# Optimization experiments

Measured on AMD Instinct MI355X. Metric: run time of the kernel, lower is better.

The kernel has to match this reference:

```python
import jax, jax.numpy as jnp
import numpy as np

NUM_SEGMENTS = 16

def setup_inputs() -> dict:
    key = jax.random.key(0)
    k1, k2, k3, k4 = jax.random.split(key, 4)
    C, R = 256, 4
    x = jax.random.normal(k1, (1000000, C), dtype=jnp.float32)
    indices = jax.random.randint(k2, (1000000,), 0, NUM_SEGMENTS, dtype=jnp.int64)
    # Linear weights (torch Linear: y = x @ W.T); store as (in, out) for einsum
    w1 = jax.random.normal(k3, (C, C // R), dtype=jnp.float32) / np.sqrt(C)
    w2 = jax.random.normal(k4, (C // R, C), dtype=jnp.float32) / np.sqrt(C // R)
    return {"x": x, "indices": indices, "w1": w1, "w2": w2}

def reference(x, indices, w1, w2):
    idx = indices.astype(jnp.int32)
    # scatter-mean over segments: (S, C)
    seg_sum = jax.ops.segment_sum(x, idx, num_segments=NUM_SEGMENTS)
    counts = jax.ops.segment_sum(jnp.ones((x.shape[0],), x.dtype), idx, num_segments=NUM_SEGMENTS)
    seg_mean = seg_sum / jnp.maximum(counts, 1.0)[:, None]
    # tiny SE MLP: Linear -> ReLU -> Linear -> Sigmoid
    h = jax.nn.relu(seg_mean @ w1)
    gate = jax.nn.sigmoid(h @ w2)  # (S, C)
    # gather per-point gate and modulate
    return x * gate[idx]
```

## Files before the change

### kernel.cpp

```cpp
#include <hip/hip_runtime.h>
#include <math.h>

#define C 256
#define S 16
#define CR 64
#define NREP 16

typedef float f4 __attribute__((ext_vector_type(4)));

__global__ __launch_bounds__(256) void k_hist(
    const int* __restrict__ idx, int* __restrict__ pcnt, int nrows)
{
    const int lane = threadIdx.x & 63;
    const int tid  = blockIdx.x * blockDim.x + threadIdx.x;
    const int T    = gridDim.x * blockDim.x;
    const int padded = ((nrows + 63) >> 6) << 6;

    int c0=0,c1=0,c2=0,c3=0,c4=0,c5=0,c6=0,c7=0,
        c8=0,c9=0,c10=0,c11=0,c12=0,c13=0,c14=0,c15=0;

    for (int i = tid; i < padded; i += T) {
        const int v = (i < nrows) ? idx[i] : -1;
        #define CNT(K) c##K += (int)__popcll(__ballot(v == K));
        CNT(0)  CNT(1)  CNT(2)  CNT(3)  CNT(4)  CNT(5)  CNT(6)  CNT(7)
        CNT(8)  CNT(9)  CNT(10) CNT(11) CNT(12) CNT(13) CNT(14) CNT(15)
        #undef CNT
    }
    if (lane == 0) {
        #define FL(K) if (c##K) atomicAdd(&pcnt[K], c##K);
        FL(0)  FL(1)  FL(2)  FL(3)  FL(4)  FL(5)  FL(6)  FL(7)
        FL(8)  FL(9)  FL(10) FL(11) FL(12) FL(13) FL(14) FL(15)
        #undef FL
    }
}

__global__ __launch_bounds__(256, 4) void k_segsum(
    const float* __restrict__ x, const int* __restrict__ idx,
    float* __restrict__ psum, int nrows)
{
    const int  tid = blockIdx.x * 256 + threadIdx.x;
    const int  T   = gridDim.x * 256;
    const long n4  = (long)nrows * (C / 4);

    f4 a0={0,0,0,0},a1={0,0,0,0},a2={0,0,0,0},a3={0,0,0,0},
       a4={0,0,0,0},a5={0,0,0,0},a6={0,0,0,0},a7={0,0,0,0},
       a8={0,0,0,0},a9={0,0,0,0},a10={0,0,0,0},a11={0,0,0,0},
       a12={0,0,0,0},a13={0,0,0,0},a14={0,0,0,0},a15={0,0,0,0};

    const f4* __restrict__ x4 = reinterpret_cast<const f4*>(x);

    #define ACC1(K, sv, vv) { const float m = (sv == K) ? 1.0f : 0.0f; \
        a##K.x = fmaf(m, vv.x, a##K.x); a##K.y = fmaf(m, vv.y, a##K.y); \
        a##K.z = fmaf(m, vv.z, a##K.z); a##K.w = fmaf(m, vv.w, a##K.w); }
    #define ROW(sv, vv) \
        ACC1(0,sv,vv)  ACC1(1,sv,vv)  ACC1(2,sv,vv)  ACC1(3,sv,vv) \
        ACC1(4,sv,vv)  ACC1(5,sv,vv)  ACC1(6,sv,vv)  ACC1(7,sv,vv) \
        ACC1(8,sv,vv)  ACC1(9,sv,vv)  ACC1(10,sv,vv) ACC1(11,sv,vv) \
        ACC1(12,sv,vv) ACC1(13,sv,vv) ACC1(14,sv,vv) ACC1(15,sv,vv)

    long i = tid;
    for (; i + T < n4; i += 2L * T) {
        const f4  v0 = x4[i];
        const f4  v1 = x4[i + T];
        const int s0 = idx[i >> 6];
        const int s1 = idx[(i + T) >> 6];
        ROW(s0, v0)
        ROW(s1, v1)
    }
    for (; i < n4; i += T) {
        const f4  v = x4[i];
        const int s = idx[i >> 6];
        ROW(s, v)
    }
    #undef ROW
    #undef ACC1

    __shared__ float red[4][8][C];
    const int w    = threadIdx.x >> 6;
    const int lane = threadIdx.x & 63;
    const int t    = threadIdx.x;
    const int rep  = blockIdx.x & (NREP - 1);
    float* gs = psum + (size_t)rep * S * C;

    #define ST(K, SL) *reinterpret_cast<f4*>(&red[w][SL][4 * lane]) = a##K;
    ST(0,0) ST(1,1) ST(2,2) ST(3,3) ST(4,4) ST(5,5) ST(6,6) ST(7,7)
    __syncthreads();
    #pragma unroll
    for (int s_ = 0; s_ < 8; s_++) {
        const float v = red[0][s_][t] + red[1][s_][t] +
                        red[2][s_][t] + red[3][s_][t];
        atomicAdd(&gs[s_ * C + t], v);
    }
    __syncthreads();
    ST(8,0) ST(9,1) ST(10,2) ST(11,3) ST(12,4) ST(13,5) ST(14,6) ST(15,7)
    __syncthreads();
    #pragma unroll
    for (int s_ = 0; s_ < 8; s_++) {
        const float v = red[0][s_][t] + red[1][s_][t] +
                        red[2][s_][t] + red[3][s_][t];
        atomicAdd(&gs[(8 + s_) * C + t], v);
    }
    #undef ST
}

__global__ __launch_bounds__(256) void k_mlp(
    const float* __restrict__ psum, const int* __restrict__ pcnt,
    const float* __restrict__ w1, const float* __restrict__ w2,
    float* __restrict__ gate)
{
    __shared__ float sm[S][C];
    __shared__ float h[S][CR];
    __shared__ float cnt[S];
    const int t = threadIdx.x;

    if (t < S) cnt[t] = fmaxf((float)pcnt[t], 1.0f);
    __syncthreads();

    for (int i = t; i < S * C; i += 256) {
        float v = 0.0f;
        #pragma unroll
        for (int r = 0; r < NREP; r++) v += psum[r * S * C + i];
        sm[i / C][i % C] = v / cnt[i / C];
    }
    __syncthreads();

    for (int o = t; o < S * CR; o += 256) {
        const int s = o / CR, j = o % CR;
        float acc = 0.0f;
        #pragma unroll 4
        for (int k = 0; k < C; k++) acc += sm[s][k] * w1[k * CR + j];
        h[s][j] = fmaxf(acc, 0.0f);
    }
    __syncthreads();

    for (int o = t; o < S * C; o += 256) {
        const int s = o / C, j = o % C;
        float acc = 0.0f;
        #pragma unroll
        for (int k = 0; k < CR; k++) acc += h[s][k] * w2[k * C + j];
        gate[o] = 1.0f / (1.0f + expf(-acc));
    }
}

__global__ __launch_bounds__(256) void k_mod(
    const float* __restrict__ x, const int* __restrict__ idx,
    const float* __restrict__ gate, float* __restrict__ out, int nrows)
{
    const int l    = threadIdx.x & 63;
    const int wrow = threadIdx.x >> 6;
    const float4* __restrict__ x4 = reinterpret_cast<const float4*>(x);
    const float4* __restrict__ g4 = reinterpret_cast<const float4*>(gate);
    float4* __restrict__ o4 = reinterpret_cast<float4*>(out);

    for (int row = blockIdx.x * 4 + wrow; row < nrows; row += gridDim.x * 4) {
        const int s = idx[row];
        float4 v = x4[row * (C / 4) + l];
        const float4 g = g4[s * (C / 4) + l];
        v.x *= g.x; v.y *= g.y; v.z *= g.z; v.w *= g.w;
        o4[row * (C / 4) + l] = v;
    }
}

extern "C" void kernel_launch(void* const* d_in, const int* in_sizes, int n_in,
                              void* d_out, int out_size, void* d_ws, size_t ws_size,
                              hipStream_t stream)
{
    const float* x   = (const float*)d_in[0];
    const int*   idx = (const int*)  d_in[1];
    const float* w1  = (const float*)d_in[2];
    const float* w2  = (const float*)d_in[3];
    float* out = (float*)d_out;
    const int nrows = in_sizes[1];

    float* psum = (float*)d_ws;
    int*   pcnt = (int*)(psum + NREP * S * C);
    float* gate = (float*)(pcnt + S);

    const size_t zero_bytes = NREP * S * C * sizeof(float) + S * sizeof(int);
    (void)hipMemsetAsync(d_ws, 0, zero_bytes, stream);

    k_hist  <<< 128, 256, 0, stream>>>(idx, pcnt, nrows);
    k_segsum<<<1024, 256, 0, stream>>>(x, idx, psum, nrows);
    k_mlp   <<<   1, 256, 0, stream>>>(psum, pcnt, w1, w2, gate);
    k_mod   <<<2048, 256, 0, stream>>>(x, idx, gate, out, nrows);
}
```

Baseline: 794.3 us.

## Restructure segment-sum as per-wave 64-row superblocks with double-buffered loads

The segment-sum kernel now assigns each wavefront a block of 64 consecutive rows. It loads those 64 indices once per lane and broadcasts each row's segment id with readlane, which makes the id wave-uniform (scalar) instead of a per-thread index load. Row loads are double-buffered in groups of four so memory fetches overlap the masked accumulate, and the next block's indices are prefetched. This adds register pressure from the eight buffered f4 values, and leftover rows are handled serially by a single wave.

```diff
diff --git a/kernel.cpp b/kernel.cpp
--- a/kernel.cpp
+++ b/kernel.cpp
@@ -38,9 +38,10 @@
     const float* __restrict__ x, const int* __restrict__ idx,
     float* __restrict__ psum, int nrows)
 {
-    const int  tid = blockIdx.x * 256 + threadIdx.x;
-    const int  T   = gridDim.x * 256;
-    const long n4  = (long)nrows * (C / 4);
+    const int lane = threadIdx.x & 63;
+    const int w    = threadIdx.x >> 6;
+    const int gw   = blockIdx.x * 4 + w;
+    const int nw   = gridDim.x * 4;
 
     f4 a0={0,0,0,0},a1={0,0,0,0},a2={0,0,0,0},a3={0,0,0,0},
        a4={0,0,0,0},a5={0,0,0,0},a6={0,0,0,0},a7={0,0,0,0},
@@ -58,28 +59,59 @@
         ACC1(8,sv,vv)  ACC1(9,sv,vv)  ACC1(10,sv,vv) ACC1(11,sv,vv) \
         ACC1(12,sv,vv) ACC1(13,sv,vv) ACC1(14,sv,vv) ACC1(15,sv,vv)
 
-    long i = tid;
-    for (; i + T < n4; i += 2L * T) {
-        const f4  v0 = x4[i];
-        const f4  v1 = x4[i + T];
-        const int s0 = idx[i >> 6];
-        const int s1 = idx[(i + T) >> 6];
-        ROW(s0, v0)
-        ROW(s1, v1)
-    }
-    for (; i < n4; i += T) {
-        const f4  v = x4[i];
-        const int s = idx[i >> 6];
-        ROW(s, v)
-    }
+    #define LOADG(BUF, p, J) { \
+        BUF[0] = (p)[(J+0) * (C/4)]; BUF[1] = (p)[(J+1) * (C/4)]; \
+        BUF[2] = (p)[(J+2) * (C/4)]; BUF[3] = (p)[(J+3) * (C/4)]; }
+    #define COMPG(BUF, vidx, J) { \
+        { const int s_ = __builtin_amdgcn_readlane(vidx, J+0); ROW(s_, BUF[0]) } \
+        { const int s_ = __builtin_amdgcn_readlane(vidx, J+1); ROW(s_, BUF[1]) } \
+        { const int s_ = __builtin_amdgcn_readlane(vidx, J+2); ROW(s_, BUF[2]) } \
+        { const int s_ = __builtin_amdgcn_readlane(vidx, J+3); ROW(s_, BUF[3]) } }
+
+    const int nsb = nrows >> 6;
+    int vidx = (gw < nsb) ? idx[(gw << 6) + lane] : 0;
+    for (int sb = gw; sb < nsb; sb += nw) {
+        const int row0 = sb << 6;
+        const f4* __restrict__ p = x4 + (size_t)row0 * (C/4) + lane;
+        const int sbn = sb + nw;
+        int vidx_n = vidx;
+        if (sbn < nsb) vidx_n = idx[(sbn << 6) + lane];
+
+        f4 A[4], B[4];
+        LOADG(A, p, 0)
+        LOADG(B, p, 4)   COMPG(A, vidx, 0)
+        LOADG(A, p, 8)   COMPG(B, vidx, 4)
+        LOADG(B, p, 12)  COMPG(A, vidx, 8)
+        LOADG(A, p, 16)  COMPG(B, vidx, 12)
+        LOADG(B, p, 20)  COMPG(A, vidx, 16)
+        LOADG(A, p, 24)  COMPG(B, vidx, 20)
+        LOADG(B, p, 28)  COMPG(A, vidx, 24)
+        LOADG(A, p, 32)  COMPG(B, vidx, 28)
+        LOADG(B, p, 36)  COMPG(A, vidx, 32)
+        LOADG(A, p, 40)  COMPG(B, vidx, 36)
+        LOADG(B, p, 44)  COMPG(A, vidx, 40)
+        LOADG(A, p, 48)  COMPG(B, vidx, 44)
+        LOADG(B, p, 52)  COMPG(A, vidx, 48)
+        LOADG(A, p, 56)  COMPG(B, vidx, 52)
+        LOADG(B, p, 60)  COMPG(A, vidx, 56)
+        COMPG(B, vidx, 60)
+        vidx = vidx_n;
+    }
+    if (gw == 0) {
+        for (int r = nsb << 6; r < nrows; ++r) {
+            const int sv = __builtin_amdgcn_readfirstlane(idx[r]);
+            const f4 vv = x4[(size_t)r * (C/4) + lane];
+            ROW(sv, vv)
+        }
+    }
+    #undef LOADG
+    #undef COMPG
     #undef ROW
     #undef ACC1
 
     __shared__ float red[4][8][C];
-    const int w    = threadIdx.x >> 6;
-    const int lane = threadIdx.x & 63;
-    const int t    = threadIdx.x;
-    const int rep  = blockIdx.x & (NREP - 1);
+    const int t   = threadIdx.x;
+    const int rep = blockIdx.x & (NREP - 1);
     float* gs = psum + (size_t)rep * S * C;
 
     #define ST(K, SL) *reinterpret_cast<f4*>(&red[w][SL][4 * lane]) = a##K;
```

Measured after the change: 789.5 us. About the same (-0.6%).

## Replace masked 16-way segment accumulation with counting-sort permutation and gathered sums

Applied to the files above, without the earlier changes.

Adds a scatter kernel that builds a per-segment row permutation from the histogram, using shared-memory counters plus a global cursor per segment. The segment-sum kernel then walks rows in segment order, so each wavefront keeps a single accumulator instead of 16 masked FMA accumulators. It flushes to global atomics only when a segment boundary is crossed. The aim is to remove the redundant masked arithmetic and the large shared-memory reduction. The cost is an extra kernel, perm writes and reads, and row gathers from x in non-sequential order.

```diff
diff --git a/kernel.cpp b/kernel.cpp
--- a/kernel.cpp
+++ b/kernel.cpp
@@ -34,73 +34,94 @@
     }
 }
 
-__global__ __launch_bounds__(256, 4) void k_segsum(
-    const float* __restrict__ x, const int* __restrict__ idx,
-    float* __restrict__ psum, int nrows)
-{
-    const int  tid = blockIdx.x * 256 + threadIdx.x;
-    const int  T   = gridDim.x * 256;
-    const long n4  = (long)nrows * (C / 4);
-
-    f4 a0={0,0,0,0},a1={0,0,0,0},a2={0,0,0,0},a3={0,0,0,0},
-       a4={0,0,0,0},a5={0,0,0,0},a6={0,0,0,0},a7={0,0,0,0},
-       a8={0,0,0,0},a9={0,0,0,0},a10={0,0,0,0},a11={0,0,0,0},
-       a12={0,0,0,0},a13={0,0,0,0},a14={0,0,0,0},a15={0,0,0,0};
+__global__ __launch_bounds__(256) void k_scatter(
+    const int* __restrict__ idx, const int* __restrict__ pcnt,
+    int* __restrict__ cursor, int* __restrict__ perm, int nrows)
+{
+    __shared__ int lc[S];
+    __shared__ int lb[S];
+    const int t = threadIdx.x;
+
+    int soff_t = 0;
+    if (t < S) for (int j = 0; j < t; j++) soff_t += pcnt[j];
+
+    const int nchunks = (nrows + 2047) >> 11;
+    for (int c = blockIdx.x; c < nchunks; c += gridDim.x) {
+        const int c0 = c << 11;
+        const int c1 = min(c0 + 2048, nrows);
+        if (t < S) lc[t] = 0;
+        __syncthreads();
+        for (int r = c0 + t; r < c1; r += 256) atomicAdd(&lc[idx[r]], 1);
+        __syncthreads();
+        if (t < S) lb[t] = soff_t + atomicAdd(&cursor[t], lc[t]);
+        __syncthreads();
+        for (int r = c0 + t; r < c1; r += 256) {
+            const int pos = atomicAdd(&lb[idx[r]], 1);
+            perm[pos] = r;
+        }
+        __syncthreads();
+    }
+}
+
+__global__ __launch_bounds__(256) void k_segsum(
+    const float* __restrict__ x, const int* __restrict__ perm,
+    const int* __restrict__ pcnt, float* __restrict__ psum, int nrows)
+{
+    const int lane = threadIdx.x & 63;
+    const int wid  = (blockIdx.x * blockDim.x + threadIdx.x) >> 6;
+    const int rep  = wid & (NREP - 1);
+    float* gs = psum + (size_t)rep * S * C;
+
+    int soff_mine = 0;
+    #pragma unroll
+    for (int j = 0; j < S; j++) soff_mine += (lane > j) ? pcnt[j] : 0;
+    #define SOFF(k) __shfl(soff_mine, (k))
 
     const f4* __restrict__ x4 = reinterpret_cast<const f4*>(x);
-
-    #define ACC1(K, sv, vv) { const float m = (sv == K) ? 1.0f : 0.0f; \
-        a##K.x = fmaf(m, vv.x, a##K.x); a##K.y = fmaf(m, vv.y, a##K.y); \
-        a##K.z = fmaf(m, vv.z, a##K.z); a##K.w = fmaf(m, vv.w, a##K.w); }
-    #define ROW(sv, vv) \
-        ACC1(0,sv,vv)  ACC1(1,sv,vv)  ACC1(2,sv,vv)  ACC1(3,sv,vv) \
-        ACC1(4,sv,vv)  ACC1(5,sv,vv)  ACC1(6,sv,vv)  ACC1(7,sv,vv) \
-        ACC1(8,sv,vv)  ACC1(9,sv,vv)  ACC1(10,sv,vv) ACC1(11,sv,vv) \
-        ACC1(12,sv,vv) ACC1(13,sv,vv) ACC1(14,sv,vv) ACC1(15,sv,vv)
-
-    long i = tid;
-    for (; i + T < n4; i += 2L * T) {
-        const f4  v0 = x4[i];
-        const f4  v1 = x4[i + T];
-        const int s0 = idx[i >> 6];
-        const int s1 = idx[(i + T) >> 6];
-        ROW(s0, v0)
-        ROW(s1, v1)
-    }
-    for (; i < n4; i += T) {
-        const f4  v = x4[i];
-        const int s = idx[i >> 6];
-        ROW(s, v)
-    }
-    #undef ROW
-    #undef ACC1
-
-    __shared__ float red[4][8][C];
-    const int w    = threadIdx.x >> 6;
-    const int lane = threadIdx.x & 63;
-    const int t    = threadIdx.x;
-    const int rep  = blockIdx.x & (NREP - 1);
-    float* gs = psum + (size_t)rep * S * C;
-
-    #define ST(K, SL) *reinterpret_cast<f4*>(&red[w][SL][4 * lane]) = a##K;
-    ST(0,0) ST(1,1) ST(2,2) ST(3,3) ST(4,4) ST(5,5) ST(6,6) ST(7,7)
-    __syncthreads();
-    #pragma unroll
-    for (int s_ = 0; s_ < 8; s_++) {
-        const float v = red[0][s_][t] + red[1][s_][t] +
-                        red[2][s_][t] + red[3][s_][t];
-        atomicAdd(&gs[s_ * C + t], v);
-    }
-    __syncthreads();
-    ST(8,0) ST(9,1) ST(10,2) ST(11,3) ST(12,4) ST(13,5) ST(14,6) ST(15,7)
-    __syncthreads();
-    #pragma unroll
-    for (int s_ = 0; s_ < 8; s_++) {
-        const float v = red[0][s_][t] + red[1][s_][t] +
-                        red[2][s_][t] + red[3][s_][t];
-        atomicAdd(&gs[(8 + s_) * C + t], v);
-    }
-    #undef ST
+    const int w0 = wid << 8;
+    if (w0 >= nrows) return;
+
+    f4  acc = {0, 0, 0, 0};
+    int cur = 0;
+
+    #define FLUSH() { float* fp = gs + cur * C + 4 * lane; \
+        atomicAdd(fp + 0, acc.x); atomicAdd(fp + 1, acc.y); \
+        atomicAdd(fp + 2, acc.z); atomicAdd(fp + 3, acc.w); \
+        acc.x = 0; acc.y = 0; acc.z = 0; acc.w = 0; }
+
+    #pragma unroll 1
+    for (int g = 0; g < 4; g++) {
+        const int jb = w0 + (g << 6);
+        if (jb >= nrows) break;
+        const int pv = perm[jb + lane];
+        while (jb >= SOFF(cur + 1)) { FLUSH() cur++; }
+        if (jb + 64 <= SOFF(cur + 1)) {
+            #pragma unroll
+            for (int b = 0; b < 8; b++) {
+                #define RL(K) const int r##K = __builtin_amdgcn_readlane(pv, b * 8 + K);
+                RL(0) RL(1) RL(2) RL(3) RL(4) RL(5) RL(6) RL(7)
+                #undef RL
+                const f4 v0 = x4[(size_t)r0 * 64 + lane];
+                const f4 v1 = x4[(size_t)r1 * 64 + lane];
+                const f4 v2 = x4[(size_t)r2 * 64 + lane];
+                const f4 v3 = x4[(size_t)r3 * 64 + lane];
+                const f4 v4 = x4[(size_t)r4 * 64 + lane];
+                const f4 v5 = x4[(size_t)r5 * 64 + lane];
+                const f4 v6 = x4[(size_t)r6 * 64 + lane];
+                const f4 v7 = x4[(size_t)r7 * 64 + lane];
+                acc += ((v0 + v1) + (v2 + v3)) + ((v4 + v5) + (v6 + v7));
+            }
+        } else {
+            for (int j = jb; j < jb + 64 && j < nrows; j++) {
+                while (j >= SOFF(cur + 1)) { FLUSH() cur++; }
+                const int row = __shfl(pv, j - jb);
+                acc += x4[(size_t)row * 64 + lane];
+            }
+        }
+    }
+    FLUSH()
+    #undef FLUSH
+    #undef SOFF
 }
 
 __global__ __launch_bounds__(256) void k_mlp(
@@ -172,15 +193,18 @@
     float* out = (float*)d_out;
     const int nrows = in_sizes[1];
 
-    float* psum = (float*)d_ws;
-    int*   pcnt = (int*)(psum + NREP * S * C);
-    float* gate = (float*)(pcnt + S);
-
-    const size_t zero_bytes = NREP * S * C * sizeof(float) + S * sizeof(int);
+    float* psum   = (float*)d_ws;
+    int*   pcnt   = (int*)(psum + NREP * S * C);
+    int*   cursor = pcnt + S;
+    float* gate   = (float*)(cursor + S);
+    int*   perm   = (int*)(gate + S * C);
+
+    const size_t zero_bytes = NREP * S * C * sizeof(float) + 2 * S * sizeof(int);
     (void)hipMemsetAsync(d_ws, 0, zero_bytes, stream);
 
-    k_hist  <<< 128, 256, 0, stream>>>(idx, pcnt, nrows);
-    k_segsum<<<1024, 256, 0, stream>>>(x, idx, psum, nrows);
-    k_mlp   <<<   1, 256, 0, stream>>>(psum, pcnt, w1, w2, gate);
-    k_mod   <<<2048, 256, 0, stream>>>(x, idx, gate, out, nrows);
-}
+    k_hist   <<< 128, 256, 0, stream>>>(idx, pcnt, nrows);
+    k_scatter<<< 512, 256, 0, stream>>>(idx, pcnt, cursor, perm, nrows);
+    k_segsum <<<1024, 256, 0, stream>>>(x, perm, pcnt, psum, nrows);
+    k_mlp    <<<   1, 256, 0, stream>>>(psum, pcnt, w1, w2, gate);
+    k_mod    <<<2048, 256, 0, stream>>>(x, idx, gate, out, nrows);
+}
```

Result: slower. 924.9 us (+16.4%).

## Restructure segment-sum into row superblocks with f2 columns and readlane indices

Applied to the files above, without the earlier changes.

The segment-sum kernel now processes 64-row superblocks per block. Each pair of waves covers half a row's columns as float2, and the segment index comes from one coalesced idx load broadcast with readlane. Eight rows' loads are batched per step, the accumulators shrink to f2 to allow 8 blocks per CU, and the grid grows to 4096 blocks. The aim is to remove the per-element idx gathers and raise memory-level parallelism. The cost is more blocks flushing atomics into the partial-sum replicas, plus narrower 8-byte loads.

```diff
diff --git a/kernel.cpp b/kernel.cpp
--- a/kernel.cpp
+++ b/kernel.cpp
@@ -6,6 +6,7 @@
 #define CR 64
 #define NREP 16
 
+typedef float f2 __attribute__((ext_vector_type(2)));
 typedef float f4 __attribute__((ext_vector_type(4)));
 
 __global__ __launch_bounds__(256) void k_hist(
@@ -34,61 +35,71 @@
     }
 }
 
-__global__ __launch_bounds__(256, 4) void k_segsum(
+__global__ __launch_bounds__(256, 8) void k_segsum(
     const float* __restrict__ x, const int* __restrict__ idx,
     float* __restrict__ psum, int nrows)
 {
-    const int  tid = blockIdx.x * 256 + threadIdx.x;
-    const int  T   = gridDim.x * 256;
-    const long n4  = (long)nrows * (C / 4);
+    const int lane = threadIdx.x & 63;
+    const int w    = threadIdx.x >> 6;
+    const int half = w & 1;
+    const int span = (w >> 1) << 5;
 
-    f4 a0={0,0,0,0},a1={0,0,0,0},a2={0,0,0,0},a3={0,0,0,0},
-       a4={0,0,0,0},a5={0,0,0,0},a6={0,0,0,0},a7={0,0,0,0},
-       a8={0,0,0,0},a9={0,0,0,0},a10={0,0,0,0},a11={0,0,0,0},
-       a12={0,0,0,0},a13={0,0,0,0},a14={0,0,0,0},a15={0,0,0,0};
+    f2 a0={0,0},a1={0,0},a2={0,0},a3={0,0},a4={0,0},a5={0,0},a6={0,0},a7={0,0},
+       a8={0,0},a9={0,0},a10={0,0},a11={0,0},a12={0,0},a13={0,0},a14={0,0},a15={0,0};
 
-    const f4* __restrict__ x4 = reinterpret_cast<const f4*>(x);
+    const f2* __restrict__ x2 = reinterpret_cast<const f2*>(x);
 
     #define ACC1(K, sv, vv) { const float m = (sv == K) ? 1.0f : 0.0f; \
-        a##K.x = fmaf(m, vv.x, a##K.x); a##K.y = fmaf(m, vv.y, a##K.y); \
-        a##K.z = fmaf(m, vv.z, a##K.z); a##K.w = fmaf(m, vv.w, a##K.w); }
+        a##K.x = fmaf(m, vv.x, a##K.x); a##K.y = fmaf(m, vv.y, a##K.y); }
     #define ROW(sv, vv) \
         ACC1(0,sv,vv)  ACC1(1,sv,vv)  ACC1(2,sv,vv)  ACC1(3,sv,vv) \
         ACC1(4,sv,vv)  ACC1(5,sv,vv)  ACC1(6,sv,vv)  ACC1(7,sv,vv) \
         ACC1(8,sv,vv)  ACC1(9,sv,vv)  ACC1(10,sv,vv) ACC1(11,sv,vv) \
         ACC1(12,sv,vv) ACC1(13,sv,vv) ACC1(14,sv,vv) ACC1(15,sv,vv)
 
-    long i = tid;
-    for (; i + T < n4; i += 2L * T) {
-        const f4  v0 = x4[i];
-        const f4  v1 = x4[i + T];
-        const int s0 = idx[i >> 6];
-        const int s1 = idx[(i + T) >> 6];
-        ROW(s0, v0)
-        ROW(s1, v1)
+    const int nsb = nrows >> 6;
+    for (int sb = blockIdx.x; sb < nsb; sb += gridDim.x) {
+        const int row0 = sb << 6;
+        const int vidx = idx[row0 + lane];
+        const f2* __restrict__ p =
+            x2 + (size_t)(row0 + span) * 128 + half * 64 + lane;
+        #pragma unroll 1
+        for (int j = 0; j < 32; j += 8) {
+            f2  v[8];
+            int s[8];
+            #pragma unroll
+            for (int k = 0; k < 8; k++)
+                v[k] = p[(size_t)(j + k) * 128];
+            #pragma unroll
+            for (int k = 0; k < 8; k++)
+                s[k] = __builtin_amdgcn_readlane(vidx, span + j + k);
+            #pragma unroll
+            for (int k = 0; k < 8; k++) { ROW(s[k], v[k]) }
+        }
     }
-    for (; i < n4; i += T) {
-        const f4  v = x4[i];
-        const int s = idx[i >> 6];
-        ROW(s, v)
+    if (blockIdx.x == 0 && span == 0) {
+        for (int r = nsb << 6; r < nrows; ++r) {
+            const int sv = __builtin_amdgcn_readfirstlane(idx[r]);
+            const f2 vv = x2[(size_t)r * 128 + half * 64 + lane];
+            ROW(sv, vv)
+        }
     }
     #undef ROW
     #undef ACC1
 
-    __shared__ float red[4][8][C];
-    const int w    = threadIdx.x >> 6;
-    const int lane = threadIdx.x & 63;
+    __shared__ float red[2][8][C];
+    const int rg   = w >> 1;
+    const int coff = half * 128 + 2 * lane;
     const int t    = threadIdx.x;
-    const int rep  = blockIdx.x & (NREP - 1);
+    const int rep  = (blockIdx.x * 4 + w) & (NREP - 1);
     float* gs = psum + (size_t)rep * S * C;
 
-    #define ST(K, SL) *reinterpret_cast<f4*>(&red[w][SL][4 * lane]) = a##K;
+    #define ST(K, SL) *reinterpret_cast<f2*>(&red[rg][SL][coff]) = a##K;
     ST(0,0) ST(1,1) ST(2,2) ST(3,3) ST(4,4) ST(5,5) ST(6,6) ST(7,7)
     __syncthreads();
     #pragma unroll
     for (int s_ = 0; s_ < 8; s_++) {
-        const float v = red[0][s_][t] + red[1][s_][t] +
-                        red[2][s_][t] + red[3][s_][t];
+        const float v = red[0][s_][t] + red[1][s_][t];
         atomicAdd(&gs[s_ * C + t], v);
     }
     __syncthreads();
@@ -96,8 +107,7 @@
     __syncthreads();
     #pragma unroll
     for (int s_ = 0; s_ < 8; s_++) {
-        const float v = red[0][s_][t] + red[1][s_][t] +
-                        red[2][s_][t] + red[3][s_][t];
+        const float v = red[0][s_][t] + red[1][s_][t];
         atomicAdd(&gs[(8 + s_) * C + t], v);
     }
     #undef ST
@@ -180,7 +190,7 @@
     (void)hipMemsetAsync(d_ws, 0, zero_bytes, stream);
 
     k_hist  <<< 128, 256, 0, stream>>>(idx, pcnt, nrows);
-    k_segsum<<<1024, 256, 0, stream>>>(x, idx, psum, nrows);
+    k_segsum<<<4096, 256, 0, stream>>>(x, idx, psum, nrows);
     k_mlp   <<<   1, 256, 0, stream>>>(psum, pcnt, w1, w2, gate);
     k_mod   <<<2048, 256, 0, stream>>>(x, idx, gate, out, nrows);
 }
```

After: 812.0 us. +2.2%, slower.
